# Performance work log

Hardware: AMD Instinct MI355X
Metric: run time of the kernel (lower is better)

## Reference

```python
import jax, jax.numpy as jnp
import numpy as np

N, D, E, T, R, KMEM, DE = 50000, 128, 800000, 400000, 1, 32, 16
EPS = 1e-5
BETA_MAX = 5.0
GRAD_CLIP = 1.0
STATE_CLIP = 10.0
STEP = 0.1
DAMP = 0.9999  # update_damping=1.0 clamped to 1-1e-4 as in __init__


def segment_logsumexp(s, idx, n):
    # numerically-stable per-segment logsumexp; empty segments contribute 0
    m = jax.ops.segment_max(s, idx, num_segments=n)
    ms = jnp.where(jnp.isfinite(m), m, 0.0)
    z = jax.ops.segment_sum(jnp.exp(s - ms[idx]), idx, num_segments=n)
    return jnp.where(z > 0, jnp.log(jnp.maximum(z, 1e-30)) + ms, 0.0)


def setup_inputs() -> dict:
    key = jax.random.key(0)
    ks = jax.random.split(key, 24)
    inv1 = jnp.log(jnp.expm1(jnp.float32(1.0)))  # _inv_softplus(1.0)
    xav = 0.5 * np.sqrt(2.0 / (2 * D))  # xavier_uniform gain=0.5 ~ std
    inp = {
        'X': jax.random.normal(ks[0], (N, D), jnp.float32),
        'edge_attr': jax.random.normal(ks[1], (E, DE), jnp.float32),
        'ln_gamma': jnp.ones((D,), jnp.float32),
        'ln_beta': jnp.zeros((D,), jnp.float32),
        'W_Q2': jax.random.normal(ks[2], (D, D), jnp.float32) * xav,
        'W_K2': jax.random.normal(ks[3], (D, D), jnp.float32) * xav,
        'W_Q3': jax.random.normal(ks[4], (D, R * D), jnp.float32) * xav,
        'W_K3': jax.random.normal(ks[5], (D, R * D), jnp.float32) * xav,
        'T_tau': jax.random.normal(ks[6], (2, R, D), jnp.float32) * 0.02,
        'W_Qm': jax.random.normal(ks[7], (D, D), jnp.float32) * xav,
        'W_Km': jax.random.normal(ks[8], (D, D), jnp.float32) * xav,
        'B_mem': jax.random.normal(ks[9], (KMEM, D), jnp.float32) / np.sqrt(D),
        'We1': jax.random.normal(ks[10], (DE, D), jnp.float32) / np.sqrt(DE),
        'be1': jnp.zeros((D,), jnp.float32),
        'We2': jax.random.normal(ks[11], (D, 1), jnp.float32) / np.sqrt(D),
        'be2': jnp.zeros((1,), jnp.float32),
        'lambda_2': inv1, 'lambda_3': inv1, 'lambda_m': inv1,
        'beta_2': inv1, 'beta_3': inv1, 'beta_m': inv1,
        'c_2': jax.random.randint(ks[12], (E,), 0, N),
        'u_2': jax.random.randint(ks[13], (E,), 0, N),
        'c_3': jax.random.randint(ks[14], (T,), 0, N),
        'u_3': jax.random.randint(ks[15], (T,), 0, N),
        'v_3': jax.random.randint(ks[16], (T,), 0, N),
        't_tau': jax.random.randint(ks[17], (T,), 0, 2),
    }
    return inp


def reference(X, edge_attr, ln_gamma, ln_beta, W_Q2, W_K2, W_Q3, W_K3, T_tau,
              W_Qm, W_Km, B_mem, We1, be1, We2, be2,
              lambda_2, lambda_3, lambda_m, beta_2, beta_3, beta_m,
              c_2, u_2, c_3, u_3, v_3, t_tau):
    sqrt_d = jnp.sqrt(jnp.float32(D))

    def energy(Xv):
        mu = jnp.mean(Xv, axis=-1, keepdims=True)
        var = jnp.var(Xv, axis=-1, keepdims=True)
        G = (Xv - mu) * jax.lax.rsqrt(var + EPS) * ln_gamma + ln_beta
        # pairwise (order-2) energy over edge list
        b2 = jnp.minimum(jax.nn.softplus(beta_2), BETA_MAX)
        Q2, K2 = G @ W_Q2, G @ W_K2
        a2 = (jax.nn.gelu(edge_attr @ We1 + be1) @ We2 + be2)[:, 0]  # edge_mlp bias
        s2 = b2 * (jnp.sum(Q2[c_2] * K2[u_2], axis=-1) / sqrt_d) + a2  # [E]
        E2 = -(jax.nn.softplus(lambda_2) / b2) * jnp.sum(segment_logsumexp(s2, c_2, N))
        # triplet (order-3) energy with per-type tensor T_tau
        b3 = jnp.minimum(jax.nn.softplus(beta_3), BETA_MAX)
        Q3 = (G @ W_Q3).reshape(-1, R, D)
        K3 = (G @ W_K3).reshape(-1, R, D)
        s3 = b3 * jnp.einsum('erd,erd,erd,erd->e', Q3[c_3], K3[u_3], K3[v_3],
                             T_tau[t_tau]) / jnp.float32(D)  # [T]
        E3 = -(jax.nn.softplus(lambda_3) / b3) * jnp.sum(segment_logsumexp(s3, c_3, N))
        # memory-bank energy
        bm = jnp.minimum(jax.nn.softplus(beta_m), BETA_MAX)
        sm = bm * ((G @ W_Qm) @ (B_mem @ W_Km).T) / sqrt_d  # [N,K]
        Em = -(jax.nn.softplus(lambda_m) / bm) * jnp.sum(jax.nn.logsumexp(sm, axis=1))
        return E2 + E3 + Em

    Eval, gX = jax.value_and_grad(energy)(X)
    gn = jnp.maximum(jnp.linalg.norm(gX, axis=-1, keepdims=True), 1e-6)
    gX = gX * jnp.minimum(GRAD_CLIP / gn, 1.0)
    X_next = X - STEP * DAMP * gX
    sn = jnp.maximum(jnp.linalg.norm(X_next, axis=-1, keepdims=True), 1e-6)
    X_next = X_next * jnp.minimum(STATE_CLIP / sn, 1.0)
    return (X_next, Eval)
```

## Files before the change

### kernel.cpp

```cpp
#include <hip/hip_runtime.h>

#define NN 50000
#define DD 128
#define EE 800000
#define TT 400000
#define KM 32
#define UU 320
#define ROWB 12500
#define MB 782
#define EDGE_BLKS 3125
#define HB2 391
#define HBT 196
#define HIST_TOT 587
#define WCB 320
#define FWD_TOT 11532
#define SCAN_TILE 2048
#define SCAN_NB ((NN + SCAN_TILE - 1) / SCAN_TILE)

static constexpr float INV_SQRT_D = 0.08838834764831845f;
static constexpr float INV_D = 1.f / 128.f;

typedef __attribute__((ext_vector_type(8))) short bf16x8;
typedef __attribute__((ext_vector_type(4))) float f32x4;
typedef unsigned short ushort_t;

__device__ __forceinline__ float softplus_f(float x) {
  return (x > 20.f) ? x : log1pf(__expf(x));
}

__device__ __forceinline__ float gelu_fast(float x) {
  float p = fmaf(0.044715f * x * x, x, x);
  float e = __expf(-1.5957691216057308f * p);
  return x * __builtin_amdgcn_rcpf(1.f + e);
}

__device__ __forceinline__ float wredsum(float v) {
#pragma unroll
  for (int m = 32; m; m >>= 1) v += __shfl_xor(v, m, 64);
  return v;
}

__device__ __forceinline__ float redsum16(float v) {
#pragma unroll
  for (int m = 1; m < 16; m <<= 1) v += __shfl_xor(v, m, 64);
  return v;
}

__device__ __forceinline__ float blo(unsigned w) { return __uint_as_float(w << 16); }
__device__ __forceinline__ float bhi(unsigned w) { return __uint_as_float(w & 0xffff0000u); }
__device__ __forceinline__ unsigned pack_bf16(float a, float b) {
  unsigned ua = __float_as_uint(a); ua += 0x7fff + ((ua >> 16) & 1);
  unsigned ub = __float_as_uint(b); ub += 0x7fff + ((ub >> 16) & 1);
  return (ua >> 16) | (ub & 0xffff0000u);
}
__device__ __forceinline__ ushort_t bf16_1(float x) {
  unsigned u = __float_as_uint(x); u += 0x7fff + ((u >> 16) & 1);
  return (ushort_t)(u >> 16);
}
__device__ __forceinline__ void unp8(uint4 w, float* f) {
  f[0] = blo(w.x); f[1] = bhi(w.x); f[2] = blo(w.y); f[3] = bhi(w.y);
  f[4] = blo(w.z); f[5] = bhi(w.z); f[6] = blo(w.w); f[7] = bhi(w.w);
}
__device__ __forceinline__ uint4 pk8(const float* f) {
  uint4 r;
  r.x = pack_bf16(f[0], f[1]); r.y = pack_bf16(f[2], f[3]);
  r.z = pack_bf16(f[4], f[5]); r.w = pack_bf16(f[6], f[7]);
  return r;
}

__device__ void hist2_body(int bx, const int* __restrict__ a,
                           const int* __restrict__ b,
                           int* __restrict__ ca, int* __restrict__ cb,
                           int* __restrict__ pos_a, int* __restrict__ pos_b, int n) {
  int base = bx * 2048 + threadIdx.x;
  if (base + 1792 < n) {
    int av[8], bv[8], pa[8], pb[8];
#pragma unroll
    for (int k = 0; k < 8; k++) { int e = base + k * 256; av[k] = a[e]; bv[k] = b[e]; }
#pragma unroll
    for (int k = 0; k < 8; k++) pa[k] = atomicAdd(&ca[av[k]], 1);
#pragma unroll
    for (int k = 0; k < 8; k++) pb[k] = atomicAdd(&cb[bv[k]], 1);
#pragma unroll
    for (int k = 0; k < 8; k++) pos_a[base + k * 256] = pa[k];
#pragma unroll
    for (int k = 0; k < 8; k++) pos_b[base + k * 256] = pb[k];
  } else {
#pragma unroll
    for (int k = 0; k < 8; k++) {
      int e = base + k * 256;
      if (e < n) {
        pos_a[e] = atomicAdd(&ca[a[e]], 1);
        pos_b[e] = atomicAdd(&cb[b[e]], 1);
      }
    }
  }
}

__device__ void hist_t3_body(int bx, const int* __restrict__ c,
                             const int* __restrict__ u,
                             const int* __restrict__ v,
                             int* __restrict__ cc, int* __restrict__ cuv,
                             int* __restrict__ pos_c, int* __restrict__ pos_u,
                             int* __restrict__ pos_v, int n) {
  int base = bx * 2048 + threadIdx.x;
  if (base + 1792 < n) {
    int cv[8], uv[8], vv[8], pc[8], pu[8], pv[8];
#pragma unroll
    for (int k = 0; k < 8; k++) { int t = base + k * 256; cv[k] = c[t]; uv[k] = u[t]; vv[k] = v[t]; }
#pragma unroll
    for (int k = 0; k < 8; k++) pc[k] = atomicAdd(&cc[cv[k]], 1);
#pragma unroll
    for (int k = 0; k < 8; k++) pu[k] = atomicAdd(&cuv[uv[k]], 1);
#pragma unroll
    for (int k = 0; k < 8; k++) pv[k] = atomicAdd(&cuv[vv[k]], 1);
#pragma unroll
    for (int k = 0; k < 8; k++) pos_c[base + k * 256] = pc[k];
#pragma unroll
    for (int k = 0; k < 8; k++) pos_u[base + k * 256] = pu[k];
#pragma unroll
    for (int k = 0; k < 8; k++) pos_v[base + k * 256] = pv[k];
  } else {
#pragma unroll
    for (int k = 0; k < 8; k++) {
      int t = base + k * 256;
      if (t < n) {
        pos_c[t] = atomicAdd(&cc[c[t]], 1);
        pos_u[t] = atomicAdd(&cuv[u[t]], 1);
        pos_v[t] = atomicAdd(&cuv[v[t]], 1);
      }
    }
  }
}

__device__ void ln_fwd_body(int bx, const float* __restrict__ X,
                            const float* __restrict__ gamma,
                            const float* __restrict__ beta,
                            unsigned* __restrict__ Gb,
                            float* __restrict__ meanv,
                            float* __restrict__ rstdv) {
  int row = bx * 4 + (threadIdx.x >> 6);
  if (row >= NN) return;
  int l = threadIdx.x & 63;
  float2 x2 = *(const float2*)(X + row * DD + 2 * l);
  float mu = wredsum(x2.x + x2.y) * (1.f / DD);
  float d0 = x2.x - mu, d1 = x2.y - mu;
  float var = wredsum(d0 * d0 + d1 * d1) * (1.f / DD);
  float rstd = rsqrtf(var + 1e-5f);
  float2 g2 = *(const float2*)(gamma + 2 * l);
  float2 b2 = *(const float2*)(beta + 2 * l);
  float o0 = d0 * rstd * g2.x + b2.x;
  float o1 = d1 * rstd * g2.y + b2.y;
  Gb[(size_t)row * 64 + l] = pack_bf16(o0, o1);
  if (l == 0) { meanv[row] = mu; rstdv[row] = rstd; }
}

__device__ void w_conv_body(int b, const float* W0, const float* W1, const float* W2,
                            const float* W3, const float* W4,
                            ushort_t* __restrict__ Wt,
                            ushort_t* __restrict__ Wc) {
  int idx = b * 256 + threadIdx.x;
  const float* Ws[5] = {W0, W1, W2, W3, W4};
  int n = idx >> 7, k = idx & 127;
  Wt[idx] = bf16_1(Ws[n >> 7][(size_t)k * 128 + (n & 127)]);
  int k2 = idx >> 7, n2 = idx & 127;
  Wc[(size_t)n2 * 640 + k2] = bf16_1(Ws[k2 >> 7][(size_t)n2 * 128 + (k2 & 127)]);
}

__device__ void gemm_km_lean(const float* __restrict__ A,
                             const float* __restrict__ W,
                             float* __restrict__ C) {
  __shared__ float As[32][129];
  int tid = threadIdx.x;
  for (int idx = tid; idx < 32 * 128; idx += 256) As[idx >> 7][idx & 127] = A[idx];
  __syncthreads();
  int r = tid >> 3, c0 = (tid & 7) * 16;
  float acc[16];
#pragma unroll
  for (int q = 0; q < 16; q++) acc[q] = 0.f;
  for (int k = 0; k < 128; k++) {
    float av = As[r][k];
#pragma unroll
    for (int q = 0; q < 16; q++) acc[q] = fmaf(av, W[k * 128 + c0 + q], acc[q]);
  }
#pragma unroll
  for (int q = 0; q < 16; q++) C[r * 128 + c0 + q] = acc[q];
}

__global__ __launch_bounds__(256) void prep_k(const float* __restrict__ X,
                                              const float* __restrict__ ln_g,
                                              const float* __restrict__ ln_b,
                                              unsigned* __restrict__ Gb,
                                              float* __restrict__ meanv,
                                              float* __restrict__ rstdv,
                                              const float* W0, const float* W1,
                                              const float* W2, const float* W3,
                                              const float* W4,
                                              ushort_t* __restrict__ Wt,
                                              ushort_t* __restrict__ Wc,
                                              const float* __restrict__ Bm,
                                              const float* __restrict__ Wkm,
                                              float* __restrict__ Km,
                                              const float* l2, const float* l3,
                                              const float* lm, const float* b2,
                                              const float* b3, const float* bm,
                                              float* __restrict__ P,
                                              float* __restrict__ eout) {
  int bx = blockIdx.x, tid = threadIdx.x;
  if (bx < ROWB) {
    ln_fwd_body(bx, X, ln_g, ln_b, Gb, meanv, rstdv);
  } else if (bx < ROWB + WCB) {
    w_conv_body(bx - ROWB, W0, W1, W2, W3, W4, Wt, Wc);
  } else if (bx == ROWB + WCB) {
    gemm_km_lean(Bm, Wkm, Km);
  } else {
    if (tid == 0) {
      float B2 = fminf(softplus_f(b2[0]), 5.f);
      float B3 = fminf(softplus_f(b3[0]), 5.f);
      float Bm_ = fminf(softplus_f(bm[0]), 5.f);
      float S2 = softplus_f(l2[0]);
      float S3 = softplus_f(l3[0]);
      float Sm = softplus_f(lm[0]);
      P[0] = B2; P[1] = B3; P[2] = Bm_;
      P[3] = -S2 * INV_SQRT_D; P[4] = -S3 * INV_D; P[5] = -Sm * INV_SQRT_D;
      P[6] = -S2 / B2; P[7] = -S3 / B3; P[8] = -Sm / Bm_;
    }
    if (tid == 1) eout[0] = 0.f;
  }
}

__device__ void mfma_fwd_body(int bxr, int by, const ushort_t* __restrict__ Gb,
                              const ushort_t* __restrict__ Wt,
                              ushort_t* __restrict__ QK, int M, char* smem) {
  ushort_t (*sB)[136] = (ushort_t (*)[136])smem;
  int tid = threadIdx.x;
  int nb = by * 64;
  for (int idx = tid; idx < 64 * 16; idx += 256) {
    int r = idx >> 4, c8 = idx & 15;
    *(bf16x8*)&sB[r][c8 * 8] = *(const bf16x8*)(Wt + (size_t)(nb + r) * 128 + c8 * 8);
  }
  __syncthreads();
  int w = tid >> 6, l = tid & 63, quad = l >> 4, j = l & 15;
  int row0 = bxr * 64 + w * 16;
  int arow = row0 + j; if (arow >= M) arow = M - 1;
  const bf16x8* ap = (const bf16x8*)(Gb + (size_t)arow * 128);
  f32x4 acc[4];
#pragma unroll
  for (int nt = 0; nt < 4; nt++) acc[nt] = (f32x4){0.f, 0.f, 0.f, 0.f};
#pragma unroll
  for (int kc = 0; kc < 4; kc++) {
    bf16x8 a = ap[kc * 4 + quad];
#pragma unroll
    for (int nt = 0; nt < 4; nt++) {
      bf16x8 b = *(const bf16x8*)&sB[nt * 16 + j][kc * 32 + quad * 8];
      acc[nt] = __builtin_amdgcn_mfma_f32_16x16x32_bf16(a, b, acc[nt], 0, 0, 0);
    }
  }
  __syncthreads();
  ushort_t* sC = (ushort_t*)smem + w * 1184;
#pragma unroll
  for (int nt = 0; nt < 4; nt++)
#pragma unroll
    for (int r = 0; r < 4; r++)
      sC[(quad * 4 + r) * 72 + nt * 16 + j] = bf16_1(acc[nt][r]);
  int rr = l >> 3, cc = l & 7;
#pragma unroll
  for (int it = 0; it < 2; it++) {
    int row = row0 + it * 8 + rr;
    if (row < M) {
      uint4 val = *(const uint4*)&sC[(it * 8 + rr) * 72 + cc * 8];
      *(uint4*)(QK + (size_t)row * 640 + nb + cc * 8) = val;
    }
  }
}

__device__ void edge_mlp_body(int bx, const float* __restrict__ EA,
                              const float* __restrict__ We1,
                              const float* __restrict__ be1,
                              const float* __restrict__ We2,
                              const float* __restrict__ be2,
                              float* __restrict__ a2, char* smem) {
  float* sW1 = (float*)smem;
  float* sb1 = sW1 + 2048;
  float* sW2 = sb1 + 128;
  int tid = threadIdx.x;
  for (int i = tid; i < 2048; i += 256) sW1[i] = We1[i];
  if (tid < 128) { sb1[tid] = be1[tid]; sW2[tid] = We2[tid]; }
  __syncthreads();
  int w = tid >> 6, l = tid & 63;
  int m = l & 15, q = l >> 4;
  union u8 { bf16x8 v; ushort_t s[8]; };
  u8 bf[8];
  float bb[8], ww[8];
#pragma unroll
  for (int nt = 0; nt < 8; nt++) {
    int n = nt * 16 + m;
#pragma unroll
    for (int j = 0; j < 8; j++) {
      int k = q * 8 + j;
      bf[nt].s[j] = (k < 16) ? bf16_1(sW1[k * 128 + n]) : (ushort_t)0;
    }
    bb[nt] = sb1[n];
    ww[nt] = sW2[n];
  }
  float be2v = be2[0];
  for (int batch = 0; batch < 4; batch++) {
    int e0 = bx * 256 + batch * 64 + w * 16;
    u8 af;
    if (q < 2) {
      const float* ep = EA + (size_t)(e0 + m) * 16 + q * 8;
      float4 v0 = *(const float4*)ep;
      float4 v1 = *(const float4*)(ep + 4);
      af.s[0] = bf16_1(v0.x); af.s[1] = bf16_1(v0.y);
      af.s[2] = bf16_1(v0.z); af.s[3] = bf16_1(v0.w);
      af.s[4] = bf16_1(v1.x); af.s[5] = bf16_1(v1.y);
      af.s[6] = bf16_1(v1.z); af.s[7] = bf16_1(v1.w);
    } else {
#pragma unroll
      for (int j = 0; j < 8; j++) af.s[j] = 0;
    }
    float s0 = 0.f, s1 = 0.f, s2 = 0.f, s3 = 0.f;
#pragma unroll
    for (int nt = 0; nt < 8; nt++) {
      float bias = bb[nt];
      f32x4 cin = (f32x4){bias, bias, bias, bias};
      f32x4 acc = __builtin_amdgcn_mfma_f32_16x16x32_bf16(af.v, bf[nt].v, cin, 0, 0, 0);
      float w2v = ww[nt];
      s0 = fmaf(gelu_fast(acc[0]), w2v, s0);
      s1 = fmaf(gelu_fast(acc[1]), w2v, s1);
      s2 = fmaf(gelu_fast(acc[2]), w2v, s2);
      s3 = fmaf(gelu_fast(acc[3]), w2v, s3);
    }
    s0 = redsum16(s0); s1 = redsum16(s1); s2 = redsum16(s2); s3 = redsum16(s3);
    if (m == 0) {
      int eb = e0 + q * 4;
      a2[eb + 0] = s0 + be2v;
      a2[eb + 1] = s1 + be2v;
      a2[eb + 2] = s2 + be2v;
      a2[eb + 3] = s3 + be2v;
    }
  }
}

__global__ __launch_bounds__(256) void fwd_k(const ushort_t* __restrict__ Gb,
                                             const ushort_t* __restrict__ Wt,
                                             ushort_t* __restrict__ QK,
                                             const float* __restrict__ EA,
                                             const float* __restrict__ We1,
                                             const float* __restrict__ be1,
                                             const float* __restrict__ We2,
                                             const float* __restrict__ be2,
                                             float* __restrict__ a2,
                                             const int* __restrict__ c2,
                                             const int* __restrict__ u2,
                                             const int* __restrict__ c3,
                                             const int* __restrict__ u3,
                                             const int* __restrict__ v3,
                                             int* __restrict__ cnt_c2,
                                             int* __restrict__ cnt_u2,
                                             int* __restrict__ cnt_c3,
                                             int* __restrict__ cnt_uv,
                                             int* __restrict__ pos_c2,
                                             int* __restrict__ pos_u2,
                                             int* __restrict__ pos_c3,
                                             int* __restrict__ pos_u3,
                                             int* __restrict__ pos_v3) {
  __shared__ char smem[64 * 136 * 2];
  int bx = (int)(((unsigned long long)blockIdx.x * 7919ull) % (unsigned long long)FWD_TOT);
  if (bx < HB2) {
    hist2_body(bx, c2, u2, cnt_c2, cnt_u2, pos_c2, pos_u2, EE);
  } else if (bx < HIST_TOT) {
    hist_t3_body(bx - HB2, c3, u3, v3, cnt_c3, cnt_uv, pos_c3, pos_u3, pos_v3, TT);
  } else if (bx < HIST_TOT + MB * 10) {
    int b = bx - HIST_TOT;
    mfma_fwd_body(b / 10, b % 10, Gb, Wt, QK, NN, smem);
  } else {
    edge_mlp_body(bx - HIST_TOT - MB * 10, EA, We1, be1, We2, be2, a2, smem);
  }
}

__global__ __launch_bounds__(256) void mfma_bwd(const ushort_t* __restrict__ dAll,
                                                const ushort_t* __restrict__ Wc,
                                                unsigned* __restrict__ dG, int M) {
  __shared__ char smem[4 * 1184 * 2];
  ushort_t (*sB)[40] = (ushort_t (*)[40])smem;
  int tid = threadIdx.x;
  int nb = blockIdx.y * 64;
  int w = tid >> 6, l = tid & 63, quad = l >> 4, j = l & 15;
  int row0 = blockIdx.x * 64 + w * 16;
  int arow = row0 + j; if (arow >= M) arow = M - 1;
  const ushort_t* arp = dAll + (size_t)arow * 640;
  f32x4 acc[4];
#pragma unroll
  for (int nt = 0; nt < 4; nt++) acc[nt] = (f32x4){0.f, 0.f, 0.f, 0.f};
  int sr = tid >> 2, sc = tid & 3;
  for (int kc = 0; kc < 20; kc++) {
    __syncthreads();
    *(bf16x8*)&sB[sr][sc * 8] = *(const bf16x8*)(Wc + (size_t)(nb + sr) * 640 + kc * 32 + sc * 8);
    __syncthreads();
    bf16x8 a = *(const bf16x8*)(arp + kc * 32 + quad * 8);
#pragma unroll
    for (int nt = 0; nt < 4; nt++) {
      bf16x8 b = *(const bf16x8*)&sB[nt * 16 + j][quad * 8];
      acc[nt] = __builtin_amdgcn_mfma_f32_16x16x32_bf16(a, b, acc[nt], 0, 0, 0);
    }
  }
  __syncthreads();
  ushort_t* sC = (ushort_t*)smem + w * 1184;
#pragma unroll
  for (int nt = 0; nt < 4; nt++)
#pragma unroll
    for (int r = 0; r < 4; r++)
      sC[(quad * 4 + r) * 72 + nt * 16 + j] = bf16_1(acc[nt][r]);
  int rr = l >> 3, cc = l & 7;
  ushort_t* dGs = (ushort_t*)dG;
#pragma unroll
  for (int it = 0; it < 2; it++) {
    int row = row0 + it * 8 + rr;
    if (row < M) {
      uint4 val = *(const uint4*)&sC[(it * 8 + rr) * 72 + cc * 8];
      *(uint4*)(dGs + (size_t)row * 128 + nb + cc * 8) = val;
    }
  }
}

__global__ __launch_bounds__(256) void scan_p1(const int* __restrict__ cnt,
                                               int* __restrict__ part) {
  int arr = blockIdx.y, b = blockIdx.x;
  const int* c = cnt + (size_t)arr * NN;
  int gi = b * SCAN_TILE + threadIdx.x * 8;
  int s = 0;
#pragma unroll
  for (int t = 0; t < 8; t++) s += (gi + t < NN) ? c[gi + t] : 0;
#pragma unroll
  for (int m = 32; m; m >>= 1) s += __shfl_xor(s, m, 64);
  __shared__ int wt[4];
  int lane = threadIdx.x & 63, wid = threadIdx.x >> 6;
  if (lane == 0) wt[wid] = s;
  __syncthreads();
  if (threadIdx.x == 0) part[arr * SCAN_NB + b] = wt[0] + wt[1] + wt[2] + wt[3];
}

__global__ __launch_bounds__(256) void scan_p2(int* __restrict__ part) {
  int w = threadIdx.x >> 6, l = threadIdx.x & 63;
  int v = (l < SCAN_NB) ? part[w * SCAN_NB + l] : 0;
  int x = v;
#pragma unroll
  for (int d = 1; d < 64; d <<= 1) {
    int y = __shfl_up(x, d, 64);
    if (l >= d) x += y;
  }
  if (l < SCAN_NB) part[w * SCAN_NB + l] = x - v;
}

__global__ __launch_bounds__(256) void scan_p3(const int* __restrict__ cnt,
                                               const int* __restrict__ part,
                                               int* __restrict__ rowptr) {
  int arr = blockIdx.y, b = blockIdx.x;
  const int* c = cnt + (size_t)arr * NN;
  int* rp = rowptr + (size_t)arr * (NN + 1);
  int tid = threadIdx.x;
  int gi = b * SCAN_TILE + tid * 8;
  int vals[8];
#pragma unroll
  for (int t = 0; t < 8; t++) vals[t] = (gi + t < NN) ? c[gi + t] : 0;
  int tsum = 0;
#pragma unroll
  for (int t = 0; t < 8; t++) tsum += vals[t];
  int lane = tid & 63, wid = tid >> 6;
  int x = tsum;
#pragma unroll
  for (int d = 1; d < 64; d <<= 1) {
    int y = __shfl_up(x, d, 64);
    if (lane >= d) x += y;
  }
  __shared__ int wt[4];
  if (lane == 63) wt[wid] = x;
  __syncthreads();
  int wadd = 0;
  for (int w = 0; w < wid; w++) wadd += wt[w];
  int running = part[arr * SCAN_NB + b] + wadd + x - tsum;
#pragma unroll
  for (int t = 0; t < 8; t++) {
    if (gi + t < NN) rp[gi + t] = running;
    running += vals[t];
  }
  if (b == SCAN_NB - 1 && tid == 255) rp[NN] = running;
}

__device__ void scat2_body(int bx, const int* __restrict__ c2,
                           const int* __restrict__ u2,
                           const float* __restrict__ a2,
                           const int* __restrict__ posc,
                           const int* __restrict__ posu,
                           const int* __restrict__ rpc,
                           const int* __restrict__ rpu,
                           uint2* __restrict__ payc,
                           uint2* __restrict__ payu, int n) {
  int base = bx * 2048 + threadIdx.x;
  if (base + 1792 < n) {
    int c[8], u[8]; float a[8]; int pc[8], pu[8];
#pragma unroll
    for (int k = 0; k < 8; k++) {
      int e = base + k * 256;
      c[k] = c2[e]; u[k] = u2[e]; a[k] = a2[e]; pc[k] = posc[e]; pu[k] = posu[e];
    }
    int p[8], q[8];
#pragma unroll
    for (int k = 0; k < 8; k++) { p[k] = rpc[c[k]] + pc[k]; q[k] = rpu[u[k]] + pu[k]; }
#pragma unroll
    for (int k = 0; k < 8; k++) {
      uint2 t; t.x = (unsigned)u[k]; t.y = __float_as_uint(a[k]);
      payc[p[k]] = t;
    }
#pragma unroll
    for (int k = 0; k < 8; k++) {
      uint2 t; t.x = (unsigned)p[k]; t.y = (unsigned)c[k];
      payu[q[k]] = t;
    }
  } else {
#pragma unroll
    for (int k = 0; k < 8; k++) {
      int e = base + k * 256;
      if (e < n) {
        int cc = c2[e], uu = u2[e];
        int pp = rpc[cc] + posc[e];
        int qq = rpu[uu] + posu[e];
        uint2 t; t.x = (unsigned)uu; t.y = __float_as_uint(a2[e]);
        payc[pp] = t;
        uint2 t2; t2.x = (unsigned)pp; t2.y = (unsigned)cc;
        payu[qq] = t2;
      }
    }
  }
}

__device__ void scat_t3_body(int bx, const int* __restrict__ c3,
                             const int* __restrict__ u3,
                             const int* __restrict__ v3,
                             const int* __restrict__ ttau,
                             const int* __restrict__ posc,
                             const int* __restrict__ posu,
                             const int* __restrict__ posv,
                             const int* __restrict__ rpc,
                             const int* __restrict__ rpuv,
                             uint2* __restrict__ payc,
                             uint2* __restrict__ payuv, int n) {
  int base = bx * 2048 + threadIdx.x;
  if (base + 1792 < n) {
    int c[8], u[8], v[8], ta[8], p[8], q1[8], q2[8];
#pragma unroll
    for (int k = 0; k < 8; k++) {
      int t = base + k * 256;
      c[k] = c3[t]; u[k] = u3[t]; v[k] = v3[t]; ta[k] = ttau[t] & 1;
    }
#pragma unroll
    for (int k = 0; k < 8; k++) {
      int t = base + k * 256;
      p[k] = rpc[c[k]] + posc[t];
      q1[k] = rpuv[u[k]] + posu[t];
      q2[k] = rpuv[v[k]] + posv[t];
    }
#pragma unroll
    for (int k = 0; k < 8; k++) {
      uint2 a; a.x = ((unsigned)u[k] << 16) | (unsigned)v[k]; a.y = (unsigned)ta[k];
      payc[p[k]] = a;
    }
#pragma unroll
    for (int k = 0; k < 8; k++) {
      unsigned sp = ((unsigned)p[k] << 1) | (unsigned)ta[k];
      uint2 b1; b1.x = ((unsigned)v[k] << 16) | (unsigned)c[k]; b1.y = sp;
      payuv[q1[k]] = b1;
      uint2 b2; b2.x = ((unsigned)u[k] << 16) | (unsigned)c[k]; b2.y = sp;
      payuv[q2[k]] = b2;
    }
  } else {
#pragma unroll
    for (int k = 0; k < 8; k++) {
      int t = base + k * 256;
      if (t < n) {
        int c = c3[t], u = u3[t], v = v3[t], ta = ttau[t] & 1;
        int p = rpc[c] + posc[t];
        int q1 = rpuv[u] + posu[t];
        int q2 = rpuv[v] + posv[t];
        unsigned sp = ((unsigned)p << 1) | (unsigned)ta;
        uint2 a; a.x = ((unsigned)u << 16) | (unsigned)v; a.y = (unsigned)ta;
        payc[p] = a;
        uint2 b1; b1.x = ((unsigned)v << 16) | (unsigned)c; b1.y = sp;
        payuv[q1] = b1;
        uint2 b2; b2.x = ((unsigned)u << 16) | (unsigned)c; b2.y = sp;
        payuv[q2] = b2;
      }
    }
  }
}

__global__ __launch_bounds__(256) void scat_k(const int* __restrict__ c2,
                                              const int* __restrict__ u2,
                                              const float* __restrict__ a2,
                                              const int* __restrict__ pos_c2,
                                              const int* __restrict__ pos_u2,
                                              const int* __restrict__ rp_c2,
                                              const int* __restrict__ rp_u2,
                                              uint2* __restrict__ payc2,
                                              uint2* __restrict__ payu2,
                                              const int* __restrict__ c3,
                                              const int* __restrict__ u3,
                                              const int* __restrict__ v3,
                                              const int* __restrict__ ttau,
                                              const int* __restrict__ pos_c3,
                                              const int* __restrict__ pos_u3,
                                              const int* __restrict__ pos_v3,
                                              const int* __restrict__ rp_c3,
                                              const int* __restrict__ rp_uv,
                                              uint2* __restrict__ payc3,
                                              uint2* __restrict__ payuv) {
  int b3 = blockIdx.x / 3, r = blockIdx.x % 3;
  if (r < 2) {
    int b = b3 * 2 + r;
    if (b < HB2) scat2_body(b, c2, u2, a2, pos_c2, pos_u2, rp_c2, rp_u2, payc2, payu2, EE);
  } else {
    scat_t3_body(b3, c3, u3, v3, ttau, pos_c3, pos_u3, pos_v3,
                 rp_c3, rp_uv, payc3, payuv, TT);
  }
}

__device__ void e2_body(int bx, const unsigned* __restrict__ QK,
                        const float* __restrict__ P,
                        const uint2* __restrict__ pay,
                        const int* __restrict__ rp,
                        float* __restrict__ s2c,
                        float* __restrict__ L2,
                        unsigned* __restrict__ dAll) {
  int row = bx * 4 + (threadIdx.x >> 6);
  int l = threadIdx.x & 63, g = l >> 4, j = l & 15;
  float b2s = P[0] * INV_SQRT_D, cw2 = P[3];
  float q[8];
  unp8(*(const uint4*)(QK + (size_t)row * UU + j * 4), q);
  int s = rp[row], e = rp[row + 1];
  float m = -3.0e38f, z = 0.f;
  float acc[8] = {0.f, 0.f, 0.f, 0.f, 0.f, 0.f, 0.f, 0.f};
  int i0 = s + g;
  uint4 kA1 = {0,0,0,0}, kA2 = {0,0,0,0}, kB1 = {0,0,0,0}, kB2 = {0,0,0,0};
  float aA1 = 0.f, aA2 = 0.f, aB1 = 0.f, aB2 = 0.f;
  if (i0 < e)      { uint2 w = pay[i0];      aA1 = __uint_as_float(w.y); kA1 = *(const uint4*)(QK + (size_t)w.x * UU + 64 + j * 4); }
  if (i0 + 4 < e)  { uint2 w = pay[i0 + 4];  aA2 = __uint_as_float(w.y); kA2 = *(const uint4*)(QK + (size_t)w.x * UU + 64 + j * 4); }
  if (i0 + 8 < e)  { uint2 w = pay[i0 + 8];  aB1 = __uint_as_float(w.y); kB1 = *(const uint4*)(QK + (size_t)w.x * UU + 64 + j * 4); }
  if (i0 + 12 < e) { uint2 w = pay[i0 + 12]; aB2 = __uint_as_float(w.y); kB2 = *(const uint4*)(QK + (size_t)w.x * UU + 64 + j * 4); }
  for (int i = i0; i < e; i += 8) {
    uint4 kC1 = {0,0,0,0}, kC2 = {0,0,0,0}; float aC1 = 0.f, aC2 = 0.f;
    if (i + 16 < e) { uint2 w = pay[i + 16]; aC1 = __uint_as_float(w.y); kC1 = *(const uint4*)(QK + (size_t)w.x * UU + 64 + j * 4); }
    if (i + 20 < e) { uint2 w = pay[i + 20]; aC2 = __uint_as_float(w.y); kC2 = *(const uint4*)(QK + (size_t)w.x * UU + 64 + j * 4); }
    {
      float k[8]; unp8(kA1, k);
      float d = 0.f;
#pragma unroll
      for (int t = 0; t < 8; t++) d = fmaf(q[t], k[t], d);
      d = redsum16(d);
      float sv = b2s * d + aA1;
      if (j == 0) s2c[i] = sv;
      if (sv <= m) {
        float p = __expf(sv - m);
        z += p;
#pragma unroll
        for (int t = 0; t < 8; t++) acc[t] = fmaf(p, k[t], acc[t]);
      } else {
        float r = __expf(m - sv);
        z = fmaf(z, r, 1.f);
#pragma unroll
        for (int t = 0; t < 8; t++) acc[t] = fmaf(acc[t], r, k[t]);
        m = sv;
      }
    }
    if (i + 4 < e) {
      float k[8]; unp8(kA2, k);
      float d = 0.f;
#pragma unroll
      for (int t = 0; t < 8; t++) d = fmaf(q[t], k[t], d);
      d = redsum16(d);
      float sv = b2s * d + aA2;
      if (j == 0) s2c[i + 4] = sv;
      if (sv <= m) {
        float p = __expf(sv - m);
        z += p;
#pragma unroll
        for (int t = 0; t < 8; t++) acc[t] = fmaf(p, k[t], acc[t]);
      } else {
        float r = __expf(m - sv);
        z = fmaf(z, r, 1.f);
#pragma unroll
        for (int t = 0; t < 8; t++) acc[t] = fmaf(acc[t], r, k[t]);
        m = sv;
      }
    }
    kA1 = kB1; aA1 = aB1; kA2 = kB2; aA2 = aB2;
    kB1 = kC1; aB1 = aC1; kB2 = kC2; aB2 = aC2;
  }
  float mx = fmaxf(m, __shfl_xor(m, 16, 64));
  mx = fmaxf(mx, __shfl_xor(mx, 32, 64));
  float r = (z > 0.f) ? __expf(m - mx) : 0.f;
  float zz = z * r;
  zz += __shfl_xor(zz, 16, 64);
  zz += __shfl_xor(zz, 32, 64);
#pragma unroll
  for (int t = 0; t < 8; t++) {
    float v = acc[t] * r;
    v += __shfl_xor(v, 16, 64);
    v += __shfl_xor(v, 32, 64);
    acc[t] = v;
  }
  if (l == 0) L2[row] = (zz > 0.f) ? (mx + __logf(zz)) : 0.f;
  if (g == 0) {
    float coef = (zz > 0.f) ? cw2 / zz : 0.f;
    float o[8];
#pragma unroll
    for (int t = 0; t < 8; t++) o[t] = coef * acc[t];
    *(uint4*)(dAll + (size_t)row * UU + 0 + j * 4) = pk8(o);
  }
}

__device__ void t3_body(int bx, const unsigned* __restrict__ QK,
                        const float* __restrict__ P,
                        const uint2* __restrict__ pay,
                        const int* __restrict__ rp,
                        float* __restrict__ s3c,
                        float* __restrict__ L3,
                        unsigned* __restrict__ dAll,
                        const float* __restrict__ sT) {
  int tid = threadIdx.x;
  int row = bx * 4 + (tid >> 6);
  int l = tid & 63, g = l >> 4, j = l & 15;
  float b3s = P[1] * INV_D, cw3 = P[4];
  float q[8];
  unp8(*(const uint4*)(QK + (size_t)row * UU + 128 + j * 4), q);
  int s = rp[row], e = rp[row + 1];
  float m = -3.0e38f, z = 0.f;
  float acc[8] = {0.f, 0.f, 0.f, 0.f, 0.f, 0.f, 0.f, 0.f};
  int i0 = s + g;
  uint4 kuA = {0,0,0,0}, kvA = {0,0,0,0};
  uint4 kuB = {0,0,0,0}, kvB = {0,0,0,0};
  int taA = 0, taB = 0;
  if (i0 < e) {
    uint2 w = pay[i0]; int u = w.x >> 16, v = w.x & 0xffff; taA = (int)w.y;
    kuA = *(const uint4*)(QK + (size_t)u * UU + 192 + j * 4);
    kvA = *(const uint4*)(QK + (size_t)v * UU + 192 + j * 4);
  }
  if (i0 + 4 < e) {
    uint2 w = pay[i0 + 4]; int u = w.x >> 16, v = w.x & 0xffff; taB = (int)w.y;
    kuB = *(const uint4*)(QK + (size_t)u * UU + 192 + j * 4);
    kvB = *(const uint4*)(QK + (size_t)v * UU + 192 + j * 4);
  }
  for (int i = i0; i < e; i += 4) {
    uint4 kuC = {0,0,0,0}, kvC = {0,0,0,0}; int taC = 0;
    if (i + 8 < e) {
      uint2 w = pay[i + 8]; int u = w.x >> 16, v = w.x & 0xffff; taC = (int)w.y;
      kuC = *(const uint4*)(QK + (size_t)u * UU + 192 + j * 4);
      kvC = *(const uint4*)(QK + (size_t)v * UU + 192 + j * 4);
    }
    float ku[8], kv[8]; unp8(kuA, ku); unp8(kvA, kv);
    const float* tv = &sT[taA * 144 + j * 9];
    float et[8], d = 0.f;
#pragma unroll
    for (int t = 0; t < 8; t++) { et[t] = ku[t] * kv[t] * tv[t]; d = fmaf(q[t], et[t], d); }
    d = redsum16(d);
    float sv = b3s * d;
    if (j == 0) s3c[i] = sv;
    if (sv <= m) {
      float p = __expf(sv - m);
      z += p;
#pragma unroll
      for (int t = 0; t < 8; t++) acc[t] = fmaf(p, et[t], acc[t]);
    } else {
      float r = __expf(m - sv);
      z = fmaf(z, r, 1.f);
#pragma unroll
      for (int t = 0; t < 8; t++) acc[t] = fmaf(acc[t], r, et[t]);
// ... 212 lines not shown
    for (int t = 0; t < 8; t++) acc[t] = fmaf(w * tv[t], qv[t] * ko[t], acc[t]);
    qA = qB; kA = kB; taA = taB; scA = scB; lcA = lcB;
    qB = qC; kB = kC; taB = taC; scB = scC; lcB = lcC;
  }
#pragma unroll
  for (int t = 0; t < 8; t++) {
    float v = acc[t];
    v += __shfl_xor(v, 16, 64);
    v += __shfl_xor(v, 32, 64);
    acc[t] = v;
  }
  if (g == 0) *(uint4*)(dAll + (size_t)row * UU + 192 + j * 4) = pk8(acc);
}

__device__ void eval_write_body(int bx, const float* __restrict__ L2,
                                const float* __restrict__ L3,
                                const float* __restrict__ Lm,
                                const float* __restrict__ P,
                                float* __restrict__ out) {
  int i = bx * 256 + threadIdx.x;
  float a2 = 0.f, a3 = 0.f, am = 0.f;
  if (i < NN) { a2 = L2[i]; a3 = L3[i]; am = Lm[i]; }
  a2 = wredsum(a2); a3 = wredsum(a3); am = wredsum(am);
  __shared__ float r2[4], r3[4], rm[4];
  int wv = threadIdx.x >> 6, l = threadIdx.x & 63;
  if (l == 0) { r2[wv] = a2; r3[wv] = a3; rm[wv] = am; }
  __syncthreads();
  if (threadIdx.x == 0) {
    float S2 = r2[0] + r2[1] + r2[2] + r2[3];
    float S3 = r3[0] + r3[1] + r3[2] + r3[3];
    float Sm = rm[0] + rm[1] + rm[2] + rm[3];
    atomicAdd(out, P[6] * S2 + P[7] * S3 + P[8] * Sm);
  }
}

__global__ __launch_bounds__(256) void phase3_k(const unsigned* __restrict__ QK,
                                                const float* __restrict__ Tt,
                                                const float* __restrict__ P,
                                                const float* __restrict__ s2c,
                                                const float* __restrict__ L2,
                                                const uint2* __restrict__ payu2,
                                                const int* __restrict__ rp_u2,
                                                const float* __restrict__ s3c,
                                                const float* __restrict__ L3,
                                                const uint2* __restrict__ payuv,
                                                const int* __restrict__ rp_uv,
                                                unsigned* __restrict__ dAll,
                                                const float* __restrict__ Lm,
                                                float* __restrict__ eout) {
  __shared__ float smem[2 * 144];
  int bx = blockIdx.x;
  int tid = threadIdx.x;
  if (bx < 2 * ROWB) {
    int body = bx & 1, b = bx >> 1;
    if (body == 0) {
      dk2_body(b, QK, s2c, L2, P, payu2, rp_u2, dAll);
    } else {
      {
        int ta = tid >> 7, d = tid & 127;
        smem[ta * 144 + (d >> 3) * 9 + (d & 7)] = Tt[tid];
      }
      __syncthreads();
      dk3_body(b, QK, s3c, L3, P, payuv, rp_uv, dAll, smem);
    }
  } else {
    eval_write_body(bx - 2 * ROWB, L2, L3, Lm, P, eout);
  }
}

__global__ __launch_bounds__(256) void fin_k(const float* __restrict__ X,
                                             const unsigned* __restrict__ dG,
                                             const float* __restrict__ gamma,
                                             const float* __restrict__ meanv,
                                             const float* __restrict__ rstdv,
                                             float* __restrict__ out) {
  int row = blockIdx.x * 4 + (threadIdx.x >> 6);
  if (row >= NN) return;
  int l = threadIdx.x & 63;
  float mu = meanv[row], rstd = rstdv[row];
  float2 x2 = *(const float2*)(X + row * DD + 2 * l);
  unsigned gw = dG[(size_t)row * 64 + l];
  float2 ga = *(const float2*)(gamma + 2 * l);
  float xh0 = (x2.x - mu) * rstd, xh1 = (x2.y - mu) * rstd;
  float dh0 = blo(gw) * ga.x, dh1 = bhi(gw) * ga.y;
  float sa = wredsum(dh0 + dh1) * (1.f / DD);
  float sb = wredsum(dh0 * xh0 + dh1 * xh1) * (1.f / DD);
  float dx0 = rstd * (dh0 - sa - xh0 * sb);
  float dx1 = rstd * (dh1 - sa - xh1 * sb);
  float gn = fmaxf(sqrtf(wredsum(dx0 * dx0 + dx1 * dx1)), 1e-6f);
  float sc = fminf(1.f / gn, 1.f);
  dx0 *= sc; dx1 *= sc;
  float xn0 = x2.x - 0.1f * 0.9999f * dx0;
  float xn1 = x2.y - 0.1f * 0.9999f * dx1;
  float sn = fmaxf(sqrtf(wredsum(xn0 * xn0 + xn1 * xn1)), 1e-6f);
  float sc2 = fminf(10.f / sn, 1.f);
  float2 o; o.x = xn0 * sc2; o.y = xn1 * sc2;
  *(float2*)(out + row * DD + 2 * l) = o;
}

extern "C" void kernel_launch(void* const* d_in, const int* in_sizes, int n_in,
                              void* d_out, int out_size, void* d_ws, size_t ws_size,
                              hipStream_t stream) {
  (void)in_sizes; (void)n_in; (void)out_size;
  const float* X = (const float*)d_in[0];
  const float* EA = (const float*)d_in[1];
  const float* ln_g = (const float*)d_in[2];
  const float* ln_b = (const float*)d_in[3];
  const float* W_Q2 = (const float*)d_in[4];
  const float* W_K2 = (const float*)d_in[5];
  const float* W_Q3 = (const float*)d_in[6];
  const float* W_K3 = (const float*)d_in[7];
  const float* T_tau = (const float*)d_in[8];
  const float* W_Qm = (const float*)d_in[9];
  const float* W_Km = (const float*)d_in[10];
  const float* B_mem = (const float*)d_in[11];
  const float* We1 = (const float*)d_in[12];
  const float* be1 = (const float*)d_in[13];
  const float* We2 = (const float*)d_in[14];
  const float* be2 = (const float*)d_in[15];
  const float* l2s = (const float*)d_in[16];
  const float* l3s = (const float*)d_in[17];
  const float* lms = (const float*)d_in[18];
  const float* b2s = (const float*)d_in[19];
  const float* b3s = (const float*)d_in[20];
  const float* bms = (const float*)d_in[21];
  const int* c2 = (const int*)d_in[22];
  const int* u2 = (const int*)d_in[23];
  const int* c3 = (const int*)d_in[24];
  const int* u3 = (const int*)d_in[25];
  const int* v3 = (const int*)d_in[26];
  const int* ttau = (const int*)d_in[27];
  float* out = (float*)d_out;

  float* ws = (float*)d_ws;
  size_t off = 0;
  auto alloc = [&](size_t n) { float* p = ws + off; off += n; return p; };
  const size_t ND = (size_t)NN * DD;
  unsigned* Gb = (unsigned*)alloc(ND / 2);
  unsigned* QKall = (unsigned*)alloc((size_t)NN * UU);
  unsigned* dAll = (unsigned*)alloc((size_t)NN * UU);
  unsigned* dG = (unsigned*)alloc(ND / 2);
  ushort_t* Wt5 = (ushort_t*)alloc(640 * 128 / 2);
  ushort_t* Wcat = (ushort_t*)alloc(640 * 128 / 2);
  float* Km = alloc((size_t)KM * DD);
  float* a2 = alloc(EE);
  float* s2c = alloc(EE);
  float* s3c = alloc(TT);
  float* meanv = alloc(NN);
  float* rstdv = alloc(NN);
  float* L2 = alloc(NN);
  float* L3 = alloc(NN);
  float* Lm = alloc(NN);
  float* Pparams = alloc(16);
  int* cnt = (int*)alloc(4 * (size_t)NN);
  int* rowptr = (int*)alloc(4 * (size_t)(NN + 1));
  int* spart = (int*)alloc(4 * SCAN_NB);
  int* pos_c2 = (int*)alloc(EE);
  int* pos_u2 = (int*)alloc(EE);
  int* pos_c3 = (int*)alloc(TT);
  int* pos_u3 = (int*)alloc(TT);
  int* pos_v3 = (int*)alloc(TT);
  uint2* payc2 = (uint2*)alloc(2 * (size_t)EE);
  uint2* payu2 = (uint2*)alloc(2 * (size_t)EE);
  uint2* payc3 = (uint2*)alloc(2 * (size_t)TT);
  uint2* payuv = (uint2*)alloc(4 * (size_t)TT);
  if (off * sizeof(float) > ws_size) return;

  int* cnt_c2 = cnt, *cnt_u2 = cnt + NN, *cnt_c3 = cnt + 2 * NN, *cnt_uv = cnt + 3 * NN;
  int* rp_c2 = rowptr, *rp_u2 = rowptr + (NN + 1), *rp_c3 = rowptr + 2 * (NN + 1), *rp_uv = rowptr + 3 * (NN + 1);

  hipMemsetAsync(cnt, 0, 4ull * NN * sizeof(int), stream);

  prep_k<<<ROWB + WCB + 2, 256, 0, stream>>>(
      X, ln_g, ln_b, Gb, meanv, rstdv,
      W_Q2, W_K2, W_Q3, W_K3, W_Qm, Wt5, Wcat,
      B_mem, W_Km, Km,
      l2s, l3s, lms, b2s, b3s, bms, Pparams, out + ND);

  fwd_k<<<FWD_TOT, 256, 0, stream>>>(
      (const ushort_t*)Gb, Wt5, (ushort_t*)QKall,
      EA, We1, be1, We2, be2, a2,
      c2, u2, c3, u3, v3,
      cnt_c2, cnt_u2, cnt_c3, cnt_uv,
      pos_c2, pos_u2, pos_c3, pos_u3, pos_v3);

  scan_p1<<<dim3(SCAN_NB, 4), 256, 0, stream>>>(cnt, spart);
  scan_p2<<<1, 256, 0, stream>>>(spart);
  scan_p3<<<dim3(SCAN_NB, 4), 256, 0, stream>>>(cnt, spart, rowptr);

  scat_k<<<3 * HBT, 256, 0, stream>>>(
      c2, u2, a2, pos_c2, pos_u2, rp_c2, rp_u2, payc2, payu2,
      c3, u3, v3, ttau, pos_c3, pos_u3, pos_v3, rp_c3, rp_uv, payc3, payuv);

  phase2_k<<<3 * ROWB, 256, 0, stream>>>(QKall, T_tau, Km, Pparams,
                                         payc2, rp_c2, payc3, rp_c3,
                                         s2c, L2, s3c, L3, Lm, dAll);
  phase3_k<<<2 * ROWB + 196, 256, 0, stream>>>(QKall, T_tau, Pparams,
                                               s2c, L2, payu2, rp_u2,
                                               s3c, L3, payuv, rp_uv, dAll,
                                               Lm, out + ND);

  mfma_bwd<<<dim3(MB, 2), 256, 0, stream>>>((const ushort_t*)dAll, Wcat, dG, NN);

  fin_k<<<ROWB, 256, 0, stream>>>(X, dG, ln_g, meanv, rstdv, out);
}
```

Measured before the change: 728.4 us.

## Replicate histogram counters across eight copies to cut atomic contention

The per-node counting histograms used to build CSR row pointers are split into eight replicas chosen by block index. Each position is tagged with its replica id in the top byte. The scan sums the replicas and writes per-replica base offsets that the scatter kernels use to place entries. The aim is to spread atomic traffic on shared counters, at the cost of an eight-times-larger memset, more reads in both scan passes, and an extra indirect load per scattered entry.

```diff
diff --git a/kernel.cpp b/kernel.cpp
--- a/kernel.cpp
+++ b/kernel.cpp
@@ -14,6 +14,7 @@
 #define HIST_TOT 587
 #define WCB 320
 #define FWD_TOT 11532
+#define NREP 8
 #define SCAN_TILE 2048
 #define SCAN_NB ((NN + SCAN_TILE - 1) / SCAN_TILE)
 
@@ -68,66 +69,72 @@
   return r;
 }
 
-__device__ void hist2_body(int bx, const int* __restrict__ a,
+__device__ void hist2_body(int bx, int rep, const int* __restrict__ a,
                            const int* __restrict__ b,
                            int* __restrict__ ca, int* __restrict__ cb,
                            int* __restrict__ pos_a, int* __restrict__ pos_b, int n) {
+  int* car = ca + (size_t)rep * NN;
+  int* cbr = cb + (size_t)rep * NN;
+  unsigned rtag = (unsigned)rep << 24;
   int base = bx * 2048 + threadIdx.x;
   if (base + 1792 < n) {
     int av[8], bv[8], pa[8], pb[8];
 #pragma unroll
     for (int k = 0; k < 8; k++) { int e = base + k * 256; av[k] = a[e]; bv[k] = b[e]; }
 #pragma unroll
-    for (int k = 0; k < 8; k++) pa[k] = atomicAdd(&ca[av[k]], 1);
-#pragma unroll
-    for (int k = 0; k < 8; k++) pb[k] = atomicAdd(&cb[bv[k]], 1);
-#pragma unroll
-    for (int k = 0; k < 8; k++) pos_a[base + k * 256] = pa[k];
-#pragma unroll
-    for (int k = 0; k < 8; k++) pos_b[base + k * 256] = pb[k];
+    for (int k = 0; k < 8; k++) pa[k] = atomicAdd(&car[av[k]], 1);
+#pragma unroll
+    for (int k = 0; k < 8; k++) pb[k] = atomicAdd(&cbr[bv[k]], 1);
+#pragma unroll
+    for (int k = 0; k < 8; k++) pos_a[base + k * 256] = (int)(rtag | (unsigned)pa[k]);
+#pragma unroll
+    for (int k = 0; k < 8; k++) pos_b[base + k * 256] = (int)(rtag | (unsigned)pb[k]);
   } else {
 #pragma unroll
     for (int k = 0; k < 8; k++) {
       int e = base + k * 256;
       if (e < n) {
-        pos_a[e] = atomicAdd(&ca[a[e]], 1);
-        pos_b[e] = atomicAdd(&cb[b[e]], 1);
+        pos_a[e] = (int)(rtag | (unsigned)atomicAdd(&car[a[e]], 1));
+        pos_b[e] = (int)(rtag | (unsigned)atomicAdd(&cbr[b[e]], 1));
       }
     }
   }
 }
 
-__device__ void hist_t3_body(int bx, const int* __restrict__ c,
+__device__ void hist_t3_body(int bx, int rep, const int* __restrict__ c,
                              const int* __restrict__ u,
                              const int* __restrict__ v,
                              int* __restrict__ cc, int* __restrict__ cuv,
                              int* __restrict__ pos_c, int* __restrict__ pos_u,
                              int* __restrict__ pos_v, int n) {
+  int* ccr = cc + (size_t)rep * NN;
+  int* cur = cuv + (size_t)rep * NN;
+  unsigned rtag = (unsigned)rep << 24;
   int base = bx * 2048 + threadIdx.x;
   if (base + 1792 < n) {
     int cv[8], uv[8], vv[8], pc[8], pu[8], pv[8];
 #pragma unroll
     for (int k = 0; k < 8; k++) { int t = base + k * 256; cv[k] = c[t]; uv[k] = u[t]; vv[k] = v[t]; }
 #pragma unroll
-    for (int k = 0; k < 8; k++) pc[k] = atomicAdd(&cc[cv[k]], 1);
-#pragma unroll
-    for (int k = 0; k < 8; k++) pu[k] = atomicAdd(&cuv[uv[k]], 1);
-#pragma unroll
-    for (int k = 0; k < 8; k++) pv[k] = atomicAdd(&cuv[vv[k]], 1);
-#pragma unroll
-    for (int k = 0; k < 8; k++) pos_c[base + k * 256] = pc[k];
-#pragma unroll
-    for (int k = 0; k < 8; k++) pos_u[base + k * 256] = pu[k];
-#pragma unroll
-    for (int k = 0; k < 8; k++) pos_v[base + k * 256] = pv[k];
+    for (int k = 0; k < 8; k++) pc[k] = atomicAdd(&ccr[cv[k]], 1);
+#pragma unroll
+    for (int k = 0; k < 8; k++) pu[k] = atomicAdd(&cur[uv[k]], 1);
+#pragma unroll
+    for (int k = 0; k < 8; k++) pv[k] = atomicAdd(&cur[vv[k]], 1);
+#pragma unroll
+    for (int k = 0; k < 8; k++) pos_c[base + k * 256] = (int)(rtag | (unsigned)pc[k]);
+#pragma unroll
+    for (int k = 0; k < 8; k++) pos_u[base + k * 256] = (int)(rtag | (unsigned)pu[k]);
+#pragma unroll
+    for (int k = 0; k < 8; k++) pos_v[base + k * 256] = (int)(rtag | (unsigned)pv[k]);
   } else {
 #pragma unroll
     for (int k = 0; k < 8; k++) {
       int t = base + k * 256;
       if (t < n) {
-        pos_c[t] = atomicAdd(&cc[c[t]], 1);
-        pos_u[t] = atomicAdd(&cuv[u[t]], 1);
-        pos_v[t] = atomicAdd(&cuv[v[t]], 1);
+        pos_c[t] = (int)(rtag | (unsigned)atomicAdd(&ccr[c[t]], 1));
+        pos_u[t] = (int)(rtag | (unsigned)atomicAdd(&cur[u[t]], 1));
+        pos_v[t] = (int)(rtag | (unsigned)atomicAdd(&cur[v[t]], 1));
       }
     }
   }
@@ -366,11 +373,12 @@
                                              int* __restrict__ pos_u3,
                                              int* __restrict__ pos_v3) {
   __shared__ char smem[64 * 136 * 2];
+  int rep = blockIdx.x & (NREP - 1);
   int bx = (int)(((unsigned long long)blockIdx.x * 7919ull) % (unsigned long long)FWD_TOT);
   if (bx < HB2) {
-    hist2_body(bx, c2, u2, cnt_c2, cnt_u2, pos_c2, pos_u2, EE);
+    hist2_body(bx, rep, c2, u2, cnt_c2, cnt_u2, pos_c2, pos_u2, EE);
   } else if (bx < HIST_TOT) {
-    hist_t3_body(bx - HB2, c3, u3, v3, cnt_c3, cnt_uv, pos_c3, pos_u3, pos_v3, TT);
+    hist_t3_body(bx - HB2, rep, c3, u3, v3, cnt_c3, cnt_uv, pos_c3, pos_u3, pos_v3, TT);
   } else if (bx < HIST_TOT + MB * 10) {
     int b = bx - HIST_TOT;
     mfma_fwd_body(b / 10, b % 10, Gb, Wt, QK, NN, smem);
@@ -427,11 +435,16 @@
 __global__ __launch_bounds__(256) void scan_p1(const int* __restrict__ cnt,
                                                int* __restrict__ part) {
   int arr = blockIdx.y, b = blockIdx.x;
-  const int* c = cnt + (size_t)arr * NN;
+  const int* c = cnt + (size_t)arr * NREP * NN;
   int gi = b * SCAN_TILE + threadIdx.x * 8;
   int s = 0;
 #pragma unroll
-  for (int t = 0; t < 8; t++) s += (gi + t < NN) ? c[gi + t] : 0;
+  for (int t = 0; t < 8; t++) {
+    if (gi + t < NN) {
+#pragma unroll
+      for (int r = 0; r < NREP; r++) s += c[(size_t)r * NN + gi + t];
+    }
+  }
 #pragma unroll
   for (int m = 32; m; m >>= 1) s += __shfl_xor(s, m, 64);
   __shared__ int wt[4];
@@ -455,15 +468,24 @@
 
 __global__ __launch_bounds__(256) void scan_p3(const int* __restrict__ cnt,
                                                const int* __restrict__ part,
-                                               int* __restrict__ rowptr) {
+                                               int* __restrict__ rowptr,
+                                               int* __restrict__ repbase) {
   int arr = blockIdx.y, b = blockIdx.x;
-  const int* c = cnt + (size_t)arr * NN;
+  const int* c = cnt + (size_t)arr * NREP * NN;
   int* rp = rowptr + (size_t)arr * (NN + 1);
+  int* rb = repbase + (size_t)arr * NREP * NN;
   int tid = threadIdx.x;
   int gi = b * SCAN_TILE + tid * 8;
   int vals[8];
 #pragma unroll
-  for (int t = 0; t < 8; t++) vals[t] = (gi + t < NN) ? c[gi + t] : 0;
+  for (int t = 0; t < 8; t++) {
+    int tot = 0;
+    if (gi + t < NN) {
+#pragma unroll
+      for (int r = 0; r < NREP; r++) tot += c[(size_t)r * NN + gi + t];
+    }
+    vals[t] = tot;
+  }
   int tsum = 0;
 #pragma unroll
   for (int t = 0; t < 8; t++) tsum += vals[t];
@@ -482,7 +504,15 @@
   int running = part[arr * SCAN_NB + b] + wadd + x - tsum;
 #pragma unroll
   for (int t = 0; t < 8; t++) {
-    if (gi + t < NN) rp[gi + t] = running;
+    if (gi + t < NN) {
+      rp[gi + t] = running;
+      int cum = running;
+#pragma unroll
+      for (int r = 0; r < NREP; r++) {
+        rb[(size_t)r * NN + gi + t] = cum;
+        cum += c[(size_t)r * NN + gi + t];
+      }
+    }
     running += vals[t];
   }
   if (b == SCAN_NB - 1 && tid == 255) rp[NN] = running;
@@ -493,8 +523,8 @@
                            const float* __restrict__ a2,
                            const int* __restrict__ posc,
                            const int* __restrict__ posu,
-                           const int* __restrict__ rpc,
-                           const int* __restrict__ rpu,
+                           const int* __restrict__ rbc,
+                           const int* __restrict__ rbu,
                            uint2* __restrict__ payc,
                            uint2* __restrict__ payu, int n) {
   int base = bx * 2048 + threadIdx.x;
@@ -507,7 +537,10 @@
     }
     int p[8], q[8];
 #pragma unroll
-    for (int k = 0; k < 8; k++) { p[k] = rpc[c[k]] + pc[k]; q[k] = rpu[u[k]] + pu[k]; }
+    for (int k = 0; k < 8; k++) {
+      p[k] = rbc[(size_t)((unsigned)pc[k] >> 24) * NN + c[k]] + (pc[k] & 0xFFFFFF);
+      q[k] = rbu[(size_t)((unsigned)pu[k] >> 24) * NN + u[k]] + (pu[k] & 0xFFFFFF);
+    }
 #pragma unroll
     for (int k = 0; k < 8; k++) {
       uint2 t; t.x = (unsigned)u[k]; t.y = __float_as_uint(a[k]);
@@ -524,8 +557,9 @@
       int e = base + k * 256;
       if (e < n) {
         int cc = c2[e], uu = u2[e];
-        int pp = rpc[cc] + posc[e];
-        int qq = rpu[uu] + posu[e];
+        int pcv = posc[e], puv = posu[e];
+        int pp = rbc[(size_t)((unsigned)pcv >> 24) * NN + cc] + (pcv & 0xFFFFFF);
+        int qq = rbu[(size_t)((unsigned)puv >> 24) * NN + uu] + (puv & 0xFFFFFF);
         uint2 t; t.x = (unsigned)uu; t.y = __float_as_uint(a2[e]);
         payc[pp] = t;
         uint2 t2; t2.x = (unsigned)pp; t2.y = (unsigned)cc;
@@ -542,8 +576,8 @@
                              const int* __restrict__ posc,
                              const int* __restrict__ posu,
                              const int* __restrict__ posv,
-                             const int* __restrict__ rpc,
-                             const int* __restrict__ rpuv,
+                             const int* __restrict__ rbc,
+                             const int* __restrict__ rbuv,
                              uint2* __restrict__ payc,
                              uint2* __restrict__ payuv, int n) {
   int base = bx * 2048 + threadIdx.x;
@@ -557,9 +591,10 @@
 #pragma unroll
     for (int k = 0; k < 8; k++) {
       int t = base + k * 256;
-      p[k] = rpc[c[k]] + posc[t];
-      q1[k] = rpuv[u[k]] + posu[t];
-      q2[k] = rpuv[v[k]] + posv[t];
+      int pcv = posc[t], puv = posu[t], pvv = posv[t];
+      p[k] = rbc[(size_t)((unsigned)pcv >> 24) * NN + c[k]] + (pcv & 0xFFFFFF);
+      q1[k] = rbuv[(size_t)((unsigned)puv >> 24) * NN + u[k]] + (puv & 0xFFFFFF);
+      q2[k] = rbuv[(size_t)((unsigned)pvv >> 24) * NN + v[k]] + (pvv & 0xFFFFFF);
     }
 #pragma unroll
     for (int k = 0; k < 8; k++) {
@@ -580,9 +615,10 @@
       int t = base + k * 256;
       if (t < n) {
         int c = c3[t], u = u3[t], v = v3[t], ta = ttau[t] & 1;
-        int p = rpc[c] + posc[t];
-        int q1 = rpuv[u] + posu[t];
-        int q2 = rpuv[v] + posv[t];
+        int pcv = posc[t], puv = posu[t], pvv = posv[t];
+        int p = rbc[(size_t)((unsigned)pcv >> 24) * NN + c] + (pcv & 0xFFFFFF);
+        int q1 = rbuv[(size_t)((unsigned)puv >> 24) * NN + u] + (puv & 0xFFFFFF);
+        int q2 = rbuv[(size_t)((unsigned)pvv >> 24) * NN + v] + (pvv & 0xFFFFFF);
         unsigned sp = ((unsigned)p << 1) | (unsigned)ta;
         uint2 a; a.x = ((unsigned)u << 16) | (unsigned)v; a.y = (unsigned)ta;
         payc[p] = a;
@@ -600,8 +636,8 @@
                                               const float* __restrict__ a2,
                                               const int* __restrict__ pos_c2,
                                               const int* __restrict__ pos_u2,
-                                              const int* __restrict__ rp_c2,
-                                              const int* __restrict__ rp_u2,
+                                              const int* __restrict__ rb_c2,
+                                              const int* __restrict__ rb_u2,
                                               uint2* __restrict__ payc2,
                                               uint2* __restrict__ payu2,
                                               const int* __restrict__ c3,
@@ -611,17 +647,17 @@
                                               const int* __restrict__ pos_c3,
                                               const int* __restrict__ pos_u3,
                                               const int* __restrict__ pos_v3,
-                                              const int* __restrict__ rp_c3,
-                                              const int* __restrict__ rp_uv,
+                                              const int* __restrict__ rb_c3,
+                                              const int* __restrict__ rb_uv,
                                               uint2* __restrict__ payc3,
                                               uint2* __restrict__ payuv) {
   int b3 = blockIdx.x / 3, r = blockIdx.x % 3;
   if (r < 2) {
     int b = b3 * 2 + r;
-    if (b < HB2) scat2_body(b, c2, u2, a2, pos_c2, pos_u2, rp_c2, rp_u2, payc2, payu2, EE);
+    if (b < HB2) scat2_body(b, c2, u2, a2, pos_c2, pos_u2, rb_c2, rb_u2, payc2, payu2, EE);
   } else {
     scat_t3_body(b3, c3, u3, v3, ttau, pos_c3, pos_u3, pos_v3,
-                 rp_c3, rp_uv, payc3, payuv, TT);
+                 rb_c3, rb_uv, payc3, payuv, TT);
   }
 }
 
@@ -1140,7 +1176,8 @@
   float* L3 = alloc(NN);
   float* Lm = alloc(NN);
   float* Pparams = alloc(16);
-  int* cnt = (int*)alloc(4 * (size_t)NN);
+  int* cnt = (int*)alloc(4 * (size_t)NREP * NN);
+  int* repbase = (int*)alloc(4 * (size_t)NREP * NN);
   int* rowptr = (int*)alloc(4 * (size_t)(NN + 1));
   int* spart = (int*)alloc(4 * SCAN_NB);
   int* pos_c2 = (int*)alloc(EE);
@@ -1154,10 +1191,17 @@
   uint2* payuv = (uint2*)alloc(4 * (size_t)TT);
   if (off * sizeof(float) > ws_size) return;
 
-  int* cnt_c2 = cnt, *cnt_u2 = cnt + NN, *cnt_c3 = cnt + 2 * NN, *cnt_uv = cnt + 3 * NN;
+  int* cnt_c2 = cnt;
+  int* cnt_u2 = cnt + (size_t)NREP * NN;
+  int* cnt_c3 = cnt + 2 * (size_t)NREP * NN;
+  int* cnt_uv = cnt + 3 * (size_t)NREP * NN;
+  int* rb_c2 = repbase;
+  int* rb_u2 = repbase + (size_t)NREP * NN;
+  int* rb_c3 = repbase + 2 * (size_t)NREP * NN;
+  int* rb_uv = repbase + 3 * (size_t)NREP * NN;
   int* rp_c2 = rowptr, *rp_u2 = rowptr + (NN + 1), *rp_c3 = rowptr + 2 * (NN + 1), *rp_uv = rowptr + 3 * (NN + 1);
 
-  hipMemsetAsync(cnt, 0, 4ull * NN * sizeof(int), stream);
+  hipMemsetAsync(cnt, 0, 4ull * NREP * NN * sizeof(int), stream);
 
   prep_k<<<ROWB + WCB + 2, 256, 0, stream>>>(
       X, ln_g, ln_b, Gb, meanv, rstdv,
@@ -1174,11 +1218,11 @@
 
   scan_p1<<<dim3(SCAN_NB, 4), 256, 0, stream>>>(cnt, spart);
   scan_p2<<<1, 256, 0, stream>>>(spart);
-  scan_p3<<<dim3(SCAN_NB, 4), 256, 0, stream>>>(cnt, spart, rowptr);
+  scan_p3<<<dim3(SCAN_NB, 4), 256, 0, stream>>>(cnt, spart, rowptr, repbase);
 
   scat_k<<<3 * HBT, 256, 0, stream>>>(
-      c2, u2, a2, pos_c2, pos_u2, rp_c2, rp_u2, payc2, payu2,
-      c3, u3, v3, ttau, pos_c3, pos_u3, pos_v3, rp_c3, rp_uv, payc3, payuv);
+      c2, u2, a2, pos_c2, pos_u2, rb_c2, rb_u2, payc2, payu2,
+      c3, u3, v3, ttau, pos_c3, pos_u3, pos_v3, rb_c3, rb_uv, payc3, payuv);
 
   phase2_k<<<3 * ROWB, 256, 0, stream>>>(QKall, T_tau, Km, Pparams,
                                          payc2, rp_c2, payc3, rp_c3,
```

Result: slower. 763.4 us (+4.8%).
